# Optimization experiments

Hardware: AMD Instinct MI355X
Metric: run time of the kernel (lower is better)

Reference implementation:

```python
import jax, jax.numpy as jnp
import numpy as np

B, T, D, H = 4, 2048, 1024, 16
DK = D // H
LN_EPS = 1e-5


def setup_inputs() -> dict:
    key = jax.random.key(0)
    ks = jax.random.split(key, 12)
    s = 1.0 / np.sqrt(D)
    inp = {
        'x': jax.random.normal(ks[0], (B, T, D), jnp.float32),
        'Wq': jax.random.normal(ks[1], (D, D), jnp.float32) * s,
        'bq': jnp.zeros((D,), jnp.float32),
        'Wk': jax.random.normal(ks[2], (D, D), jnp.float32) * s,
        'bk': jnp.zeros((D,), jnp.float32),
        'Wv': jax.random.normal(ks[3], (D, D), jnp.float32) * s,
        'bv': jnp.zeros((D,), jnp.float32),
        'Wo': jax.random.normal(ks[4], (D, D), jnp.float32) * s,
        'bo': jnp.zeros((D,), jnp.float32),
        'ln_g': jnp.ones((D,), jnp.float32),
        'ln_b': jnp.zeros((D,), jnp.float32),
    }
    return inp


def reference(x, Wq, bq, Wk, bk, Wv, bv, Wo, bo, ln_g, ln_b):
    b, t, d = x.shape
    scale = jnp.sqrt(jnp.asarray(DK, x.dtype))
    # QKV projections -> [b, h, t, dk]
    q = (x @ Wq + bq).reshape(b, t, H, DK).transpose(0, 2, 1, 3)
    k = (x @ Wk + bk).reshape(b, t, H, DK).transpose(0, 2, 1, 3)
    v = (x @ Wv + bv).reshape(b, t, H, DK).transpose(0, 2, 1, 3)
    scores = jnp.einsum('bhqd,bhkd->bhqk', q, k) / scale  # [b,h,t,t]
    mask = jnp.tril(jnp.ones((t, t), x.dtype))[None, None]  # [1,1,t,t]
    neg = jnp.finfo(x.dtype).min
    scores = jnp.where(mask == 0, neg, scores)
    attn = jax.nn.softmax(scores, axis=-1)
    # mask-renormalize (as in the torch module)
    attn = attn * mask
    denom = attn.sum(-1, keepdims=True)
    attn = jnp.where(denom > 0, attn / denom, jnp.zeros_like(attn))
    ctx = jnp.einsum('bhqk,bhkd->bhqd', attn, v)  # [b,h,t,dk]
    ctx = ctx.transpose(0, 2, 1, 3).reshape(b, t, d)
    out = ctx @ Wo + bo
    y = out + x  # residual
    mu = y.mean(-1, keepdims=True)
    var = ((y - mu) ** 2).mean(-1, keepdims=True)
    return (y - mu) / jnp.sqrt(var + LN_EPS) * ln_g + ln_b
```

## Files before the change

### kernel.cpp

```cpp
#include <hip/hip_runtime.h>


using u16 = unsigned short;
using u32 = unsigned int;
typedef _Float16 f16x8 __attribute__((ext_vector_type(8)));
typedef _Float16 f16x2 __attribute__((ext_vector_type(2)));
typedef float f32x4 __attribute__((ext_vector_type(4)));
typedef unsigned short u16x8 __attribute__((ext_vector_type(8)));

template <bool B> struct BoolTag { static constexpr bool v = B; };

__device__ inline u16 f2h_bits(float f) {
    _Float16 h = (_Float16)f;
    return __builtin_bit_cast(u16, h);
}

__device__ __forceinline__ void gload16(const void* g, void* l) {
    __builtin_amdgcn_global_load_lds(
        (const __attribute__((address_space(1))) void*)g,
        (__attribute__((address_space(3))) void*)l, 16, 0, 0);
}

__global__ __launch_bounds__(256) void convert_x_kernel(const float* __restrict__ x,
                                                        u16* __restrict__ xb) {
    size_t i = ((size_t)blockIdx.x * 256 + threadIdx.x) * 8;
    float4 a = *(const float4*)(x + i);
    float4 b = *(const float4*)(x + i + 4);
    u16x8 o;
    o[0] = f2h_bits(a.x); o[1] = f2h_bits(a.y); o[2] = f2h_bits(a.z); o[3] = f2h_bits(a.w);
    o[4] = f2h_bits(b.x); o[5] = f2h_bits(b.y); o[6] = f2h_bits(b.z); o[7] = f2h_bits(b.w);
    *(u16x8*)(xb + i) = o;
}

__global__ __launch_bounds__(256) void convert_wt_kernel(const float* __restrict__ W,
                                                         u16* __restrict__ Wt) {
    __shared__ float ts[64][68];
    const int k0 = blockIdx.x * 64, n0 = blockIdx.y * 64;
    const int tid = threadIdx.x, rr = tid >> 3, c = tid & 7;
#pragma unroll
    for (int p = 0; p < 2; p++) {
        int k = p * 32 + rr;
        float4 u = *(const float4*)(W + (size_t)(k0 + k) * 1024 + n0 + c * 8);
        float4 w = *(const float4*)(W + (size_t)(k0 + k) * 1024 + n0 + c * 8 + 4);
        *(float4*)&ts[k][c * 8] = u;
        *(float4*)&ts[k][c * 8 + 4] = w;
    }
    __syncthreads();
#pragma unroll
    for (int p = 0; p < 2; p++) {
        int n = p * 32 + rr;
        u16 o[8];
#pragma unroll
        for (int j = 0; j < 8; j++) o[j] = f2h_bits(ts[c * 8 + j][n]);
        *(u16x8*)(Wt + (size_t)(n0 + n) * 1024 + k0 + c * 8) = *(u16x8*)o;
    }
}

template <int MODE>
__global__ __launch_bounds__(256) void gemm_bt_kernel(
    const u16* __restrict__ A, const u16* __restrict__ WtBase,
    const float* __restrict__ bias0, const float* __restrict__ bias1,
    const float* __restrict__ bias2, u16* __restrict__ outb,
    float* __restrict__ outf, const float* __restrict__ xres) {
    constexpr int Kd = 1024, Nd = 1024;
    const int z = blockIdx.z;
    const u16* W = WtBase + (size_t)z * Kd * Nd;
    u16* ob = outb + (size_t)z * 8192 * Nd;
    const float* bias = (z == 0) ? bias0 : (z == 1 ? bias1 : bias2);
    const float qscale = (MODE == 0 && z == 0) ? 0.125f : 1.0f;

    __shared__ u16 As[128 * 64];
    __shared__ u16 Bs[128 * 64];

    const int tid = threadIdx.x;
    const int lane = tid & 63;
    const int wid = tid >> 6;
    const int wr = wid >> 1, wc = wid & 1;
    const int l15 = lane & 15, lg = lane >> 4;
    const size_t row0 = (size_t)blockIdx.x * 128;
    const size_t col0 = (size_t)blockIdx.y * 128;

    const int rr = tid >> 3, c8 = tid & 7;
    const int scw = (c8 ^ (rr & 7)) * 8;

    f32x4 acc[4][4] = {};

    for (int k0 = 0; k0 < Kd; k0 += 64) {
#pragma unroll
        for (int j = 0; j < 4; j++) {
            gload16(A + (row0 + j * 32 + rr) * Kd + k0 + scw,
                    As + (j * 256 + wid * 64) * 8);
            gload16(W + (col0 + j * 32 + rr) * Kd + k0 + scw,
                    Bs + (j * 256 + wid * 64) * 8);
        }
        __syncthreads();
#pragma unroll
        for (int kk = 0; kk < 2; kk++) {
            f16x8 af[4], bf[4];
            const int kc = kk * 4 + lg;
#pragma unroll
            for (int m = 0; m < 4; m++) {
                int ra = wr * 64 + m * 16 + l15;
                af[m] = *(const f16x8*)(As + ra * 64 + (kc ^ (ra & 7)) * 8);
                int rb = wc * 64 + m * 16 + l15;
                bf[m] = *(const f16x8*)(Bs + rb * 64 + (kc ^ (rb & 7)) * 8);
            }
#pragma unroll
            for (int m = 0; m < 4; m++)
#pragma unroll
                for (int n = 0; n < 4; n++)
                    acc[m][n] = __builtin_amdgcn_mfma_f32_16x16x32_f16(
                        af[m], bf[n], acc[m][n], 0, 0, 0);
        }
        __syncthreads();
    }

#pragma unroll
    for (int m = 0; m < 4; m++) {
#pragma unroll
        for (int n = 0; n < 4; n++) {
            size_t col = col0 + wc * 64 + n * 16 + l15;
            float bb = bias[col];
#pragma unroll
            for (int r = 0; r < 4; r++) {
                size_t row = row0 + wr * 64 + m * 16 + lg * 4 + r;
                float vv = acc[m][n][r] + bb;
                if (MODE == 0) {
                    ob[row * Nd + col] = f2h_bits(vv * qscale);
                } else {
                    size_t idx = row * Nd + col;
                    outf[idx] = vv + xres[idx];
                }
            }
        }
    }
}

__global__ __launch_bounds__(256) void transpose_v_kernel(const u16* __restrict__ V,
                                                          u16* __restrict__ Vt) {
    __shared__ u16 ts[64][72];
    const int bh = blockIdx.y;
    const int b = bh >> 4, h = bh & 15;
    const int t0 = blockIdx.x * 64;
    const int tid = threadIdx.x, rr = tid >> 3, c = tid & 7;
#pragma unroll
    for (int p = 0; p < 2; p++) {
        int t = p * 32 + rr;
        *(u16x8*)&ts[t][c * 8] =
            *(const u16x8*)(V + ((size_t)b * 2048 + t0 + t) * 1024 + h * 64 + c * 8);
    }
    __syncthreads();
#pragma unroll
    for (int p = 0; p < 2; p++) {
        int d = p * 32 + rr;
        u16 o[8];
#pragma unroll
        for (int j = 0; j < 8; j++) o[j] = ts[c * 8 + j][d];
        *(u16x8*)(Vt + ((size_t)bh * 64 + d) * 2048 + t0 + c * 8) = *(u16x8*)o;
    }
}

__global__ __launch_bounds__(256) void attn_kernel(const u16* __restrict__ Q,
                                                   const u16* __restrict__ Kb,
                                                   const u16* __restrict__ Vt,
                                                   u16* __restrict__ ctx) {
    __shared__ u16 Ks[2][64 * 64];
    __shared__ u16 Vs[2][64 * 64];
    __shared__ u16 plds[4][16][72];

    const int bh = blockIdx.x;
    const int b = bh >> 4, h = bh & 15;
    const int qb = 31 - (int)blockIdx.y;
    const int tid = threadIdx.x, lane = tid & 63, wid = tid >> 6;
    const int l15 = lane & 15, lg = lane >> 4;
    const int q0w = qb * 64 + wid * 16;
    const int send = qb * 64;
    const int qq = q0w + l15;

    const int rr = tid >> 3, c8 = tid & 7;
    const int scw = (c8 ^ (rr & 7)) * 8;
    const size_t kbase = ((size_t)b * 2048) * 1024 + h * 64 + scw;
    const size_t vbase = ((size_t)bh * 64 + rr) * 2048 + scw;

    f16x8 qv0, qv1;
    {
        size_t qoff = ((size_t)b * 2048 + q0w + l15) * 1024 + h * 64 + lg * 8;
        qv0 = *(const f16x8*)(Q + qoff);
        qv1 = *(const f16x8*)(Q + qoff + 32);
    }

    const int swk0 = (lg ^ (l15 & 7)) * 8;
    const int swk1 = ((4 + lg) ^ (l15 & 7)) * 8;

    f32x4 acc[4] = {};
    float psum = 0.0f;

    auto stage = [&](int s, int bf) {
#pragma unroll
        for (int ph = 0; ph < 2; ph++) {
            gload16(Kb + kbase + (size_t)(s + ph * 32 + rr) * 1024,
                    Ks[bf] + (ph * 256 + wid * 64) * 8);
            gload16(Vt + vbase + (size_t)(ph * 32) * 2048 + s,
                    Vs[bf] + (ph * 256 + wid * 64) * 8);
        }
    };

    auto body = [&](int s, int bf, auto maskc) {
        constexpr bool MASK = decltype(maskc)::v;
        f32x4 sc4[4];
#pragma unroll
        for (int c = 0; c < 4; c++) {
            const u16* kp = Ks[bf] + (c * 16 + l15) * 64;
            f16x8 kf0 = *(const f16x8*)(kp + swk0);
            f16x8 kf1 = *(const f16x8*)(kp + swk1);
            f32x4 zz = {};
            zz = __builtin_amdgcn_mfma_f32_16x16x32_f16(kf0, qv0, zz, 0, 0, 0);
            zz = __builtin_amdgcn_mfma_f32_16x16x32_f16(kf1, qv1, zz, 0, 0, 0);
            sc4[c] = zz;
        }
#pragma unroll
        for (int c = 0; c < 4; c++) {
            float p[4];
#pragma unroll
            for (int r = 0; r < 4; r++) {
                float yv = fminf(sc4[c][r] - 2.7725887f, 9.7f);
                float e = __expf(yv);
                if (MASK) e = (s + c * 16 + lg * 4 + r <= qq) ? e : 0.0f;
                psum += e;
                p[r] = e;
            }
            uint2 w;
            w.x = __builtin_bit_cast(u32, __builtin_amdgcn_cvt_pkrtz(p[0], p[1]));
            w.y = __builtin_bit_cast(u32, __builtin_amdgcn_cvt_pkrtz(p[2], p[3]));
            *(uint2*)&plds[wid][l15][c * 16 + lg * 4] = w;
        }
        f16x8 pa0 = *(const f16x8*)&plds[wid][l15][lg * 8];
        f16x8 pa1 = *(const f16x8*)&plds[wid][l15][32 + lg * 8];
#pragma unroll
        for (int dt = 0; dt < 4; dt++) {
            const u16* vp = Vs[bf] + (dt * 16 + l15) * 64;
            f16x8 vf0 = *(const f16x8*)(vp + swk0);
            f16x8 vf1 = *(const f16x8*)(vp + swk1);
            acc[dt] = __builtin_amdgcn_mfma_f32_16x16x32_f16(pa0, vf0, acc[dt], 0, 0, 0);
            acc[dt] = __builtin_amdgcn_mfma_f32_16x16x32_f16(pa1, vf1, acc[dt], 0, 0, 0);
        }
    };

    stage(0, 0);
    int cur = 0;
    for (int s = 0; s < send; s += 64) {
        __syncthreads();
        stage(s + 64, cur ^ 1);
        body(s, cur, BoolTag<false>{});
        cur ^= 1;
    }
    __syncthreads();
    body(send, cur, BoolTag<true>{});

    psum += __shfl_xor(psum, 16);
    psum += __shfl_xor(psum, 32);
    float inv = 1.0f / psum;
    float invr[4];
#pragma unroll
    for (int r = 0; r < 4; r++) invr[r] = __shfl(inv, lg * 4 + r);

#pragma unroll
    for (int dt = 0; dt < 4; dt++)
#pragma unroll
        for (int r = 0; r < 4; r++)
            ctx[((size_t)b * 2048 + q0w + lg * 4 + r) * 1024 + h * 64 + dt * 16 + l15] =
                f2h_bits(acc[dt][r] * invr[r]);
}

__global__ __launch_bounds__(256) void ln_kernel(const float* __restrict__ y,
                                                 const float* __restrict__ g,
                                                 const float* __restrict__ bb,
                                                 float* __restrict__ out) {
    const int r = blockIdx.x, tid = threadIdx.x;
    float4 v = *(const float4*)(y + (size_t)r * 1024 + tid * 4);
    float s = v.x + v.y + v.z + v.w;
    float sq = v.x * v.x + v.y * v.y + v.z * v.z + v.w * v.w;
#pragma unroll
    for (int ofs = 1; ofs < 64; ofs <<= 1) {
        s += __shfl_xor(s, ofs);
        sq += __shfl_xor(sq, ofs);
    }
    __shared__ float as[4], aq[4];
    if ((tid & 63) == 0) { as[tid >> 6] = s; aq[tid >> 6] = sq; }
    __syncthreads();
    s = as[0] + as[1] + as[2] + as[3];
    sq = aq[0] + aq[1] + aq[2] + aq[3];
    float mu = s * (1.0f / 1024.0f);
    float var = sq * (1.0f / 1024.0f) - mu * mu;
    float rstd = rsqrtf(var + 1e-5f);
    float4 gv = *(const float4*)(g + tid * 4);
    float4 bv = *(const float4*)(bb + tid * 4);
    float4 o4;
    o4.x = (v.x - mu) * rstd * gv.x + bv.x;
    o4.y = (v.y - mu) * rstd * gv.y + bv.y;
    o4.z = (v.z - mu) * rstd * gv.z + bv.z;
    o4.w = (v.w - mu) * rstd * gv.w + bv.w;
    *(float4*)(out + (size_t)r * 1024 + tid * 4) = o4;
}

extern "C" void kernel_launch(void* const* d_in, const int* in_sizes, int n_in,
                              void* d_out, int out_size, void* d_ws, size_t ws_size,
                              hipStream_t stream) {
    const float* x  = (const float*)d_in[0];
    const float* Wq = (const float*)d_in[1];
    const float* bq = (const float*)d_in[2];
    const float* Wk = (const float*)d_in[3];
    const float* bk = (const float*)d_in[4];
    const float* Wv = (const float*)d_in[5];
    const float* bv = (const float*)d_in[6];
    const float* Wo = (const float*)d_in[7];
    const float* bo = (const float*)d_in[8];
    const float* lg = (const float*)d_in[9];
    const float* lb = (const float*)d_in[10];
    float* out = (float*)d_out;

    char* ws = (char*)d_ws;
    u16* xb = (u16*)(ws + 0);
    u16* wt = (u16*)(ws + 16777216);
    u16* q  = (u16*)(ws + 25165824);
    u16* k  = (u16*)(ws + 41943040);
    u16* v  = (u16*)(ws + 58720256);
    u16* vt = (u16*)(ws + 75497472);
    u16* cx = (u16*)(ws + 92274688);
    float* y = (float*)(ws + 109051904);

    convert_x_kernel<<<4096, 256, 0, stream>>>(x, xb);
    dim3 gw(16, 16);
    convert_wt_kernel<<<gw, 256, 0, stream>>>(Wq, wt);
    convert_wt_kernel<<<gw, 256, 0, stream>>>(Wk, wt + 1048576);
    convert_wt_kernel<<<gw, 256, 0, stream>>>(Wv, wt + 2097152);
    convert_wt_kernel<<<gw, 256, 0, stream>>>(Wo, wt + 3145728);

    gemm_bt_kernel<0><<<dim3(64, 8, 3), 256, 0, stream>>>(xb, wt, bq, bk, bv, q,
                                                          nullptr, nullptr);
    transpose_v_kernel<<<dim3(32, 64), 256, 0, stream>>>(v, vt);
    attn_kernel<<<dim3(64, 32), 256, 0, stream>>>(q, k, vt, cx);
    gemm_bt_kernel<1><<<dim3(64, 8, 1), 256, 0, stream>>>(cx, wt + 3145728, bo, bo, bo,
                                                          nullptr, y, x);
    ln_kernel<<<8192, 256, 0, stream>>>(y, lg, lb, out);
}
```

Measured before the change: 198.3 us.

## Use 256x256 double-buffered QKV GEMM and 128-query attention tiles with exp2 softmax

Replaces the QKV GEMM with a 512-thread kernel that computes 256x256 tiles, double-buffers LDS through async global-to-LDS loads, uses raised wave priority around the MFMA block, and remaps block IDs for cache locality. The attention kernel now has each wave handle 32 query rows, so every K/V tile loaded into LDS serves twice as many queries. It also folds log2(e) into the Q scale so softmax can use exp2 with a fixed clamp, and stores P in a swizzled LDS layout. The cost is more registers and LDS per block, fewer attention blocks, and an extra masked diagonal step done by only half the waves.

```diff
diff --git a/kernel.cpp b/kernel.cpp
--- a/kernel.cpp
+++ b/kernel.cpp
@@ -4,7 +4,6 @@
 using u16 = unsigned short;
 using u32 = unsigned int;
 typedef _Float16 f16x8 __attribute__((ext_vector_type(8)));
-typedef _Float16 f16x2 __attribute__((ext_vector_type(2)));
 typedef float f32x4 __attribute__((ext_vector_type(4)));
 typedef unsigned short u16x8 __attribute__((ext_vector_type(8)));
 
@@ -56,19 +55,103 @@
     }
 }
 
-template <int MODE>
-__global__ __launch_bounds__(256) void gemm_bt_kernel(
-    const u16* __restrict__ A, const u16* __restrict__ WtBase,
-    const float* __restrict__ bias0, const float* __restrict__ bias1,
-    const float* __restrict__ bias2, u16* __restrict__ outb,
-    float* __restrict__ outf, const float* __restrict__ xres) {
+__global__ __launch_bounds__(512) void gemm_qkv_kernel(
+    const u16* __restrict__ A, const u16* __restrict__ Wt,
+    const float* __restrict__ bq, const float* __restrict__ bk,
+    const float* __restrict__ bv, u16* __restrict__ qo, u16* __restrict__ ko,
+    u16* __restrict__ vo) {
+    __shared__ u16 As[2][256 * 64];
+    __shared__ u16 Bs[2][256 * 64];
+
+    const int bid = blockIdx.x;
+    const int wg = (bid & 7) * 48 + (bid >> 3);
+    const int bx = wg / 12, by = wg % 12;
+    const size_t row0 = (size_t)bx * 256;
+    const size_t col0 = (size_t)by * 256;
+    const int tid = threadIdx.x, lane = tid & 63;
+    const int wid = tid >> 6, wm = wid >> 2, wn = wid & 3;
+    const int l15 = lane & 15, lg = lane >> 4;
+    const int rr = tid >> 3, c8 = tid & 7;
+    const int scw = (c8 ^ (rr & 7)) * 8;
+
+    f32x4 acc[8][4] = {};
+
+    auto stage = [&](int kt, int p) {
+        const int k0 = kt * 64;
+#pragma unroll
+        for (int h = 0; h < 2; h++)
+#pragma unroll
+            for (int j = 0; j < 2; j++) {
+                const int rbase = h * 128 + j * 64;
+                gload16(A + (row0 + rbase + rr) * 1024 + k0 + scw,
+                        As[p] + rbase * 64 + tid * 8);
+                gload16(Wt + (col0 + rbase + rr) * 1024 + k0 + scw,
+                        Bs[p] + rbase * 64 + tid * 8);
+            }
+    };
+
+    stage(0, 0);
+    int p = 0;
+    for (int kt = 0; kt < 16; kt++) {
+        stage((kt + 1) & 15, p ^ 1);
+        asm volatile("s_waitcnt vmcnt(8)" ::: "memory");
+        __builtin_amdgcn_sched_barrier(0);
+        __builtin_amdgcn_s_barrier();
+        __builtin_amdgcn_sched_barrier(0);
+        const u16* Ab = As[p];
+        const u16* Bb = Bs[p];
+#pragma unroll
+        for (int kc = 0; kc < 2; kc++) {
+            f16x8 bf[4], af[8];
+#pragma unroll
+            for (int n = 0; n < 4; n++) {
+                int rb = wn * 64 + n * 16 + l15;
+                bf[n] = *(const f16x8*)(Bb + rb * 64 + ((kc * 4 + lg) ^ (rb & 7)) * 8);
+            }
+#pragma unroll
+            for (int m = 0; m < 8; m++) {
+                int ra = wm * 128 + m * 16 + l15;
+                af[m] = *(const f16x8*)(Ab + ra * 64 + ((kc * 4 + lg) ^ (ra & 7)) * 8);
+            }
+            __builtin_amdgcn_s_setprio(1);
+#pragma unroll
+            for (int m = 0; m < 8; m++)
+#pragma unroll
+                for (int n = 0; n < 4; n++)
+                    acc[m][n] = __builtin_amdgcn_mfma_f32_16x16x32_f16(
+                        af[m], bf[n], acc[m][n], 0, 0, 0);
+            __builtin_amdgcn_s_setprio(0);
+        }
+        __builtin_amdgcn_sched_barrier(0);
+        __builtin_amdgcn_s_barrier();
+        p ^= 1;
+    }
+
+    const int zsel = by >> 2;
+    u16* ob = zsel == 0 ? qo : (zsel == 1 ? ko : vo);
+    const float* bias = zsel == 0 ? bq : (zsel == 1 ? bk : bv);
+    const float qs = zsel == 0 ? 0.18033688f : 1.0f;
+#pragma unroll
+    for (int m = 0; m < 8; m++) {
+#pragma unroll
+        for (int n = 0; n < 4; n++) {
+            size_t col = col0 + wn * 64 + n * 16 + l15;
+            size_t colz = col & 1023;
+            float bb = bias[colz];
+#pragma unroll
+            for (int r = 0; r < 4; r++) {
+                size_t row = row0 + wm * 128 + m * 16 + lg * 4 + r;
+                ob[row * 1024 + colz] = f2h_bits((acc[m][n][r] + bb) * qs);
+            }
+        }
+    }
+}
+
+__global__ __launch_bounds__(256) void gemm_wo_kernel(
+    const u16* __restrict__ A, const u16* __restrict__ W,
+    const float* __restrict__ bias, float* __restrict__ outf,
+    const float* __restrict__ xres) {
     constexpr int Kd = 1024, Nd = 1024;
-    const int z = blockIdx.z;
-    const u16* W = WtBase + (size_t)z * Kd * Nd;
-    u16* ob = outb + (size_t)z * 8192 * Nd;
-    const float* bias = (z == 0) ? bias0 : (z == 1 ? bias1 : bias2);
-    const float qscale = (MODE == 0 && z == 0) ? 0.125f : 1.0f;
-
     __shared__ u16 As[128 * 64];
     __shared__ u16 Bs[128 * 64];
 
@@ -124,13 +207,8 @@
 #pragma unroll
             for (int r = 0; r < 4; r++) {
                 size_t row = row0 + wr * 64 + m * 16 + lg * 4 + r;
-                float vv = acc[m][n][r] + bb;
-                if (MODE == 0) {
-                    ob[row * Nd + col] = f2h_bits(vv * qscale);
-                } else {
-                    size_t idx = row * Nd + col;
-                    outf[idx] = vv + xres[idx];
-                }
+                size_t idx = row * Nd + col;
+                outf[idx] = acc[m][n][r] + bb + xres[idx];
             }
         }
     }
@@ -166,34 +244,36 @@
                                                    u16* __restrict__ ctx) {
     __shared__ u16 Ks[2][64 * 64];
     __shared__ u16 Vs[2][64 * 64];
-    __shared__ u16 plds[4][16][72];
+    __shared__ u16 Ps[8][16 * 64];
 
     const int bh = blockIdx.x;
     const int b = bh >> 4, h = bh & 15;
-    const int qb = 31 - (int)blockIdx.y;
+    const int qb = 15 - (int)blockIdx.y;
     const int tid = threadIdx.x, lane = tid & 63, wid = tid >> 6;
     const int l15 = lane & 15, lg = lane >> 4;
-    const int q0w = qb * 64 + wid * 16;
-    const int send = qb * 64;
-    const int qq = q0w + l15;
+    const int q0w = qb * 128 + wid * 32;
+    const int send = qb * 128;
 
     const int rr = tid >> 3, c8 = tid & 7;
     const int scw = (c8 ^ (rr & 7)) * 8;
     const size_t kbase = ((size_t)b * 2048) * 1024 + h * 64 + scw;
     const size_t vbase = ((size_t)bh * 64 + rr) * 2048 + scw;
 
-    f16x8 qv0, qv1;
-    {
-        size_t qoff = ((size_t)b * 2048 + q0w + l15) * 1024 + h * 64 + lg * 8;
-        qv0 = *(const f16x8*)(Q + qoff);
-        qv1 = *(const f16x8*)(Q + qoff + 32);
+    f16x8 qv[2][2];
+#pragma unroll
+    for (int qf = 0; qf < 2; qf++) {
+        size_t qoff = ((size_t)b * 2048 + q0w + qf * 16 + l15) * 1024 + h * 64 + lg * 8;
+        qv[qf][0] = *(const f16x8*)(Q + qoff);
+        qv[qf][1] = *(const f16x8*)(Q + qoff + 32);
     }
 
     const int swk0 = (lg ^ (l15 & 7)) * 8;
     const int swk1 = ((4 + lg) ^ (l15 & 7)) * 8;
-
-    f32x4 acc[4] = {};
-    float psum = 0.0f;
+    u16* Pw0 = Ps[wid * 2 + 0] + l15 * 64;
+    u16* Pw1 = Ps[wid * 2 + 1] + l15 * 64;
+
+    f32x4 acc[2][4] = {};
+    float psum[2] = {0.0f, 0.0f};
 
     auto stage = [&](int s, int bf) {
 #pragma unroll
@@ -207,42 +287,62 @@
 
     auto body = [&](int s, int bf, auto maskc) {
         constexpr bool MASK = decltype(maskc)::v;
-        f32x4 sc4[4];
+        f32x4 sc[2][4];
 #pragma unroll
         for (int c = 0; c < 4; c++) {
             const u16* kp = Ks[bf] + (c * 16 + l15) * 64;
             f16x8 kf0 = *(const f16x8*)(kp + swk0);
             f16x8 kf1 = *(const f16x8*)(kp + swk1);
-            f32x4 zz = {};
-            zz = __builtin_amdgcn_mfma_f32_16x16x32_f16(kf0, qv0, zz, 0, 0, 0);
-            zz = __builtin_amdgcn_mfma_f32_16x16x32_f16(kf1, qv1, zz, 0, 0, 0);
-            sc4[c] = zz;
-        }
-#pragma unroll
-        for (int c = 0; c < 4; c++) {
-            float p[4];
-#pragma unroll
-            for (int r = 0; r < 4; r++) {
-                float yv = fminf(sc4[c][r] - 2.7725887f, 9.7f);
-                float e = __expf(yv);
-                if (MASK) e = (s + c * 16 + lg * 4 + r <= qq) ? e : 0.0f;
-                psum += e;
-                p[r] = e;
-            }
-            uint2 w;
-            w.x = __builtin_bit_cast(u32, __builtin_amdgcn_cvt_pkrtz(p[0], p[1]));
-            w.y = __builtin_bit_cast(u32, __builtin_amdgcn_cvt_pkrtz(p[2], p[3]));
-            *(uint2*)&plds[wid][l15][c * 16 + lg * 4] = w;
-        }
-        f16x8 pa0 = *(const f16x8*)&plds[wid][l15][lg * 8];
-        f16x8 pa1 = *(const f16x8*)&plds[wid][l15][32 + lg * 8];
+#pragma unroll
+            for (int qf = 0; qf < 2; qf++) {
+                f32x4 z = {};
+                z = __builtin_amdgcn_mfma_f32_16x16x32_f16(kf0, qv[qf][0], z, 0, 0, 0);
+                z = __builtin_amdgcn_mfma_f32_16x16x32_f16(kf1, qv[qf][1], z, 0, 0, 0);
+                sc[qf][c] = z;
+            }
+        }
+#pragma unroll
+        for (int qf = 0; qf < 2; qf++) {
+            u16* Pw = qf ? Pw1 : Pw0;
+#pragma unroll
+            for (int c = 0; c < 4; c++) {
+                float pv[4];
+#pragma unroll
+                for (int r = 0; r < 4; r++) {
+                    float e = __builtin_amdgcn_exp2f(fminf(sc[qf][c][r], 15.0f));
+                    if (MASK) {
+                        int kk = s + c * 16 + lg * 4 + r;
+                        e = (kk <= q0w + qf * 16 + l15) ? e : 0.0f;
+                    }
+                    psum[qf] += e;
+                    pv[r] = e;
+                }
+                uint2 w;
+                w.x = __builtin_bit_cast(u32, __builtin_amdgcn_cvt_pkrtz(pv[0], pv[1]));
+                w.y = __builtin_bit_cast(u32, __builtin_amdgcn_cvt_pkrtz(pv[2], pv[3]));
+                int gsw = (((c * 2 + (lg >> 1)) ^ (l15 & 7)) << 3) + (lg & 1) * 4;
+                *(uint2*)(Pw + gsw) = w;
+            }
+        }
+        f16x8 pa0[2], pa1[2];
+#pragma unroll
+        for (int qf = 0; qf < 2; qf++) {
+            const u16* Pw = qf ? Pw1 : Pw0;
+            pa0[qf] = *(const f16x8*)(Pw + ((lg ^ (l15 & 7)) << 3));
+            pa1[qf] = *(const f16x8*)(Pw + (((4 + lg) ^ (l15 & 7)) << 3));
+        }
 #pragma unroll
         for (int dt = 0; dt < 4; dt++) {
             const u16* vp = Vs[bf] + (dt * 16 + l15) * 64;
             f16x8 vf0 = *(const f16x8*)(vp + swk0);
             f16x8 vf1 = *(const f16x8*)(vp + swk1);
-            acc[dt] = __builtin_amdgcn_mfma_f32_16x16x32_f16(pa0, vf0, acc[dt], 0, 0, 0);
-            acc[dt] = __builtin_amdgcn_mfma_f32_16x16x32_f16(pa1, vf1, acc[dt], 0, 0, 0);
+#pragma unroll
+            for (int qf = 0; qf < 2; qf++) {
+                acc[qf][dt] =
+                    __builtin_amdgcn_mfma_f32_16x16x32_f16(pa0[qf], vf0, acc[qf][dt], 0, 0, 0);
+                acc[qf][dt] =
+                    __builtin_amdgcn_mfma_f32_16x16x32_f16(pa1[qf], vf1, acc[qf][dt], 0, 0, 0);
+            }
         }
     };
 
@@ -255,21 +355,29 @@
         cur ^= 1;
     }
     __syncthreads();
+    stage(send + 64, cur ^ 1);
     body(send, cur, BoolTag<true>{});
-
-    psum += __shfl_xor(psum, 16);
-    psum += __shfl_xor(psum, 32);
-    float inv = 1.0f / psum;
-    float invr[4];
-#pragma unroll
-    for (int r = 0; r < 4; r++) invr[r] = __shfl(inv, lg * 4 + r);
-
-#pragma unroll
-    for (int dt = 0; dt < 4; dt++)
-#pragma unroll
-        for (int r = 0; r < 4; r++)
-            ctx[((size_t)b * 2048 + q0w + lg * 4 + r) * 1024 + h * 64 + dt * 16 + l15] =
-                f2h_bits(acc[dt][r] * invr[r]);
+    cur ^= 1;
+    __syncthreads();
+    if (wid >= 2) body(send + 64, cur, BoolTag<true>{});
+
+#pragma unroll
+    for (int qf = 0; qf < 2; qf++) {
+        psum[qf] += __shfl_xor(psum[qf], 16);
+        psum[qf] += __shfl_xor(psum[qf], 32);
+    }
+#pragma unroll
+    for (int qf = 0; qf < 2; qf++) {
+        float inv = 1.0f / psum[qf];
+#pragma unroll
+        for (int r = 0; r < 4; r++) {
+            float ir = __shfl(inv, lg * 4 + r);
+            size_t row = (size_t)b * 2048 + q0w + qf * 16 + lg * 4 + r;
+#pragma unroll
+            for (int dt = 0; dt < 4; dt++)
+                ctx[row * 1024 + h * 64 + dt * 16 + l15] = f2h_bits(acc[qf][dt][r] * ir);
+        }
+    }
 }
 
 __global__ __launch_bounds__(256) void ln_kernel(const float* __restrict__ y,
@@ -336,11 +444,9 @@
     convert_wt_kernel<<<gw, 256, 0, stream>>>(Wv, wt + 2097152);
     convert_wt_kernel<<<gw, 256, 0, stream>>>(Wo, wt + 3145728);
 
-    gemm_bt_kernel<0><<<dim3(64, 8, 3), 256, 0, stream>>>(xb, wt, bq, bk, bv, q,
-                                                          nullptr, nullptr);
+    gemm_qkv_kernel<<<384, 512, 0, stream>>>(xb, wt, bq, bk, bv, q, k, v);
     transpose_v_kernel<<<dim3(32, 64), 256, 0, stream>>>(v, vt);
-    attn_kernel<<<dim3(64, 32), 256, 0, stream>>>(q, k, vt, cx);
-    gemm_bt_kernel<1><<<dim3(64, 8, 1), 256, 0, stream>>>(cx, wt + 3145728, bo, bo, bo,
-                                                          nullptr, y, x);
+    attn_kernel<<<dim3(64, 16), 256, 0, stream>>>(q, k, vt, cx);
+    gemm_wo_kernel<<<dim3(64, 8), 256, 0, stream>>>(cx, wt + 3145728, bo, y, x);
     ln_kernel<<<8192, 256, 0, stream>>>(y, lg, lb, out);
 }
```

Measured after the change: 194.9 us. Within noise of the previous version (-1.7%).
